# Optimization experiments

Hardware: AMD Instinct MI355X
Metric: run time of the kernel (lower is better)

The kernel has to match this reference:

```python
import jax, jax.numpy as jnp
import numpy as np

HEADS = 16
IN_FEATURE = 1024
D_HEAD = IN_FEATURE // HEADS
N = 32768


def setup_inputs() -> dict:
    key = jax.random.key(0)
    ks = jax.random.split(key, 16)
    s_in = 1.0 / np.sqrt(IN_FEATURE)
    inp = {
        "Q": jax.random.normal(ks[0], (N, IN_FEATURE), jnp.float32),
        "K": jax.random.normal(ks[1], (N, IN_FEATURE), jnp.float32),
        "V": jax.random.normal(ks[2], (N, IN_FEATURE), jnp.float32),
        "lq_w": jax.random.uniform(ks[3], (D_HEAD, IN_FEATURE), jnp.float32, -s_in, s_in),
        "lq_b": jax.random.uniform(ks[4], (D_HEAD,), jnp.float32, -s_in, s_in),
        "lk1_w": jax.random.uniform(ks[5], (D_HEAD, IN_FEATURE), jnp.float32, -s_in, s_in),
        "lk1_b": jax.random.uniform(ks[6], (D_HEAD,), jnp.float32, -s_in, s_in),
        "lk2_w": jax.random.uniform(ks[7], (D_HEAD, IN_FEATURE), jnp.float32, -s_in, s_in),
        "lk2_b": jax.random.uniform(ks[8], (D_HEAD,), jnp.float32, -s_in, s_in),
        "lv1_w": jax.random.uniform(ks[9], (D_HEAD, IN_FEATURE), jnp.float32, -s_in, s_in),
        "lv1_b": jax.random.uniform(ks[10], (D_HEAD,), jnp.float32, -s_in, s_in),
        "lv2_w": jax.random.uniform(ks[11], (D_HEAD, IN_FEATURE), jnp.float32, -s_in, s_in),
        "lv2_b": jax.random.uniform(ks[12], (D_HEAD,), jnp.float32, -s_in, s_in),
        "lh_w": jax.random.uniform(ks[13], (IN_FEATURE, IN_FEATURE), jnp.float32, -s_in, s_in),
        "lh_b": jax.random.uniform(ks[14], (IN_FEATURE,), jnp.float32, -s_in, s_in),
    }
    return inp


def _linear(x, w, b):
    # torch nn.Linear: x @ w.T + b
    return x @ w.T + b


def reference(Q, K, V, lq_w, lq_b, lk1_w, lk1_b, lk2_w, lk2_b,
              lv1_w, lv1_b, lv2_w, lv2_b, lh_w, lh_b):
    # The original loops over heads but the body is loop-invariant:
    # every iteration produces the identical [N, D_HEAD] tensor.
    # Compute once and tile HEADS times (same math as the torch code).
    q = _linear(Q, lq_w, lq_b)     # [N, Dh]
    k1 = _linear(K, lk1_w, lk1_b)  # [N, Dh]
    k2 = _linear(V, lk2_w, lk2_b)
    v1 = _linear(K, lv1_w, lv1_b)
    v2 = _linear(V, lv2_w, lv2_b)

    kv1 = jnp.sum(q * k1, axis=1, keepdims=True)  # [N, 1]
    kv2 = jnp.sum(q * k2, axis=1, keepdims=True)  # [N, 1]
    m = jnp.maximum(kv1, kv2)
    e1 = jnp.exp(kv1 - m)
    e2 = jnp.exp(kv2 - m)
    denom = e1 + e2
    head = (e1 / denom) * v1 + (e2 / denom) * v2   # [N, Dh]

    concat_head = jnp.tile(head, (1, HEADS))       # [N, IN_FEATURE]
    return _linear(concat_head, lh_w, lh_b)
```

## Files before the change

### kernel.cpp

```cpp
#include <hip/hip_runtime.h>
#include <hip/hip_bf16.h>

typedef __attribute__((ext_vector_type(4))) float f32x4;
typedef __attribute__((ext_vector_type(8))) short bf16x8;

#define MFMA(a, b, c) __builtin_amdgcn_mfma_f32_16x16x32_bf16(a, b, c, 0, 0, 0)

__device__ __forceinline__ short f2bf(float f) {
    union { float f; unsigned u; } v; v.f = f;
    unsigned r = v.u + 0x7fffu + ((v.u >> 16) & 1u);
    return (short)(r >> 16);
}

__device__ __forceinline__ short f2bf_h(float f) {
    __hip_bfloat16 h = __float2bfloat16(f);
    return *reinterpret_cast<const short*>(&h);
}

__device__ __forceinline__ bf16x8 cvt8h(f32x4 a, f32x4 b) {
    bf16x8 r;
    #pragma unroll
    for (int i = 0; i < 4; ++i) {
        r[i]     = f2bf_h(a[i]);
        r[4 + i] = f2bf_h(b[i]);
    }
    return r;
}

__device__ __forceinline__ void gll16(const void* g, const void* l) {
    __builtin_amdgcn_global_load_lds(
        (const __attribute__((address_space(1))) void*)g,
        (__attribute__((address_space(3))) void*)l, 16, 0, 0);
}

#define WS_WEFF   327680
#define WS_BALL_B 786432

__global__ __launch_bounds__(256) void prep_kernel(
        const float* __restrict__ lq_w, const float* __restrict__ lk1_w,
        const float* __restrict__ lk2_w, const float* __restrict__ lv1_w,
        const float* __restrict__ lv2_w, const float* __restrict__ lh_w,
        const float* __restrict__ lq_b, const float* __restrict__ lk1_b,
        const float* __restrict__ lk2_b, const float* __restrict__ lv1_b,
        const float* __restrict__ lv2_b,
        short* __restrict__ W_frag, short* __restrict__ weff,
        float* __restrict__ b_all) {
    int t = blockIdx.x * 256 + threadIdx.x;
    if (t < 327680) {
        const int e    = t & 7;
        const int u16  = t >> 3;
        const int lane = u16 & 63;
        const int tl   = u16 >> 6;
        const int c    = tl / 20;
        const int tt   = tl - c * 20;
        const int j    = tt >> 2;
        const int wd   = tt & 3;
        const int lrow = lane & 15;
        const int lkg  = lane >> 4;
        const float* src = (j == 0) ? lq_w : (j == 1) ? lk1_w
                         : (j == 2) ? lv1_w : (j == 3) ? lk2_w : lv2_w;
        W_frag[t] = f2bf(src[(wd * 16 + lrow) * 1024 + c * 32 + lkg * 8 + e]);
    } else if (t < 393216) {
        int i = t - 327680;
        int jj = i >> 6, d = i & 63;
        float s = 0.f;
        #pragma unroll
        for (int h = 0; h < 16; ++h) s += lh_w[jj * 1024 + h * 64 + d];
        weff[i] = f2bf(s);
    } else if (t < 393536) {
        int i = t - 393216;
        int seg = i >> 6, si = i & 63;
        const float* src = (seg == 0) ? lq_b : (seg == 1) ? lk1_b
                         : (seg == 2) ? lv1_b : (seg == 3) ? lk2_b : lv2_b;
        b_all[i] = src[si];
    }
}

__global__ __launch_bounds__(256, 3) void fused_kernel(
        const float* __restrict__ Q, const float* __restrict__ K,
        const float* __restrict__ V, const short* __restrict__ W_frag,
        const float* __restrict__ b_all, const short* __restrict__ weff,
        const float* __restrict__ lh_b, float* __restrict__ out) {
    __shared__ __align__(16) char lds[49152];
    const int tid  = threadIdx.x;
    const int wid  = tid >> 6;
    const int lane = tid & 63;
    const int lrow = lane & 15;
    const int lkg  = lane >> 4;
    const int RB   = blockIdx.x * 32;

    const float* asrc[3];
    int adst[3];
    #pragma unroll
    for (int u = 0; u < 3; ++u) {
        const int i   = wid * 3 + u;
        const int inp = i >> 2;
        const int rg  = i & 3;
        const int row = rg * 8 + (lane >> 3);
        const int gc  = (lane & 7) ^ (row & 7);
        const float* base = (inp == 0) ? Q : (inp == 1) ? K : V;
        asrc[u] = base + (size_t)(RB + row) * 1024 + gc * 4;
        adst[u] = inp * 4096 + rg * 1024;
    }

    const short* wsrc[5];
    #pragma unroll
    for (int j = 0; j < 5; ++j)
        wsrc[j] = W_frag + (size_t)((j * 4 + wid) * 64 + lane) * 8;

    f32x4 acc[2][5];
    #pragma unroll
    for (int rt = 0; rt < 2; ++rt)
        #pragma unroll
        for (int j = 0; j < 5; ++j) acc[rt][j] = (f32x4){0.f, 0.f, 0.f, 0.f};

    bf16x8 wE[5], wO[5];
    const int r7 = lrow & 7;
    const int c0 = ((lkg * 2)     ^ r7) << 4;
    const int c1 = ((lkg * 2 + 1) ^ r7) << 4;

#define GLD4(dst, p) \
    asm volatile("global_load_dwordx4 %0, %1, off" : "=&v"(dst) : "v"(p) : "memory")

    #pragma unroll
    for (int u = 0; u < 3; ++u) gll16(asrc[u], lds + adst[u]);
    #pragma unroll
    for (int j = 0; j < 5; ++j) GLD4(wE[j], wsrc[j]);
    #pragma unroll
    for (int u = 0; u < 3; ++u) gll16(asrc[u] + 32, lds + 12288 + adst[u]);
    #pragma unroll
    for (int j = 0; j < 5; ++j) GLD4(wO[j], wsrc[j] + 10240);
    #pragma unroll
    for (int u = 0; u < 3; ++u) gll16(asrc[u] + 64, lds + 24576 + adst[u]);
    asm volatile("s_waitcnt vmcnt(11)" ::: "memory");
    __builtin_amdgcn_sched_barrier(0);
    __builtin_amdgcn_s_barrier();
    __builtin_amdgcn_sched_barrier(0);

#define BODY(C, WB)                                                            \
    {                                                                          \
        const char* Ab = lds + ((C) & 3) * 12288;                              \
        bf16x8 fq[2], fk[2], fv[2];                                            \
        _Pragma("unroll")                                                      \
        for (int rt = 0; rt < 2; ++rt) {                                       \
            const int ro = (rt * 16 + lrow) * 128;                             \
            f32x4 q0 = *(const f32x4*)(Ab + ro + c0);                          \
            f32x4 q1 = *(const f32x4*)(Ab + ro + c1);                          \
            f32x4 k0 = *(const f32x4*)(Ab + 4096 + ro + c0);                   \
            f32x4 k1 = *(const f32x4*)(Ab + 4096 + ro + c1);                   \
            f32x4 v0 = *(const f32x4*)(Ab + 8192 + ro + c0);                   \
            f32x4 v1 = *(const f32x4*)(Ab + 8192 + ro + c1);                   \
            fq[rt] = cvt8h(q0, q1);                                            \
            fk[rt] = cvt8h(k0, k1);                                            \
            fv[rt] = cvt8h(v0, v1);                                            \
        }                                                                      \
        _Pragma("unroll")                                                      \
        for (int rt = 0; rt < 2; ++rt) {                                       \
            acc[rt][0] = MFMA(fq[rt], WB[0], acc[rt][0]);                      \
            acc[rt][1] = MFMA(fk[rt], WB[1], acc[rt][1]);                      \
            acc[rt][2] = MFMA(fk[rt], WB[2], acc[rt][2]);                      \
            acc[rt][3] = MFMA(fv[rt], WB[3], acc[rt][3]);                      \
            acc[rt][4] = MFMA(fv[rt], WB[4], acc[rt][4]);                      \
        }                                                                      \
        __builtin_amdgcn_sched_barrier(0);                                     \
           \
        const int kw = ((C) + 2 <= 31) ? (C) + 2 : 31;                         \
        _Pragma("unroll")                                                      \
        for (int j = 0; j < 5; ++j) GLD4(WB[j], wsrc[j] + kw * 10240);         \
               \
        const int ka = ((C) + 3 <= 31) ? (C) + 3 : 31;                         \
        char* Db = lds + (((C) + 3) & 3) * 12288;                              \
        _Pragma("unroll")                                                      \
        for (int u = 0; u < 3; ++u) gll16(asrc[u] + ka * 32, Db + adst[u]);    \
        __builtin_amdgcn_sched_barrier(0);                                     \
        asm volatile("s_waitcnt vmcnt(11)" ::: "memory");                      \
        __builtin_amdgcn_sched_barrier(0);                                     \
        __builtin_amdgcn_s_barrier();                                          \
        __builtin_amdgcn_sched_barrier(0);                                     \
    }

    #pragma unroll 1
    for (int cc = 0; cc < 32; cc += 2) {
        BODY(cc, wE)
        BODY(cc + 1, wO)
    }
#undef BODY
#undef GLD4

    asm volatile("s_waitcnt vmcnt(0)" ::: "memory");
    __builtin_amdgcn_sched_barrier(0);
    __syncthreads();

    float* epi = (float*)lds;
    #pragma unroll
    for (int rt = 0; rt < 2; ++rt)
        #pragma unroll
        for (int j = 0; j < 5; ++j) {
            const int col = j * 64 + wid * 16 + lrow;
            const float bb = b_all[col];
            #pragma unroll
            for (int i = 0; i < 4; ++i)
                epi[(rt * 16 + lkg * 4 + i) * 324 + col] = acc[rt][j][i] + bb;
        }
    __syncthreads();

    const int r = tid >> 3;
    const int p = tid & 7;
    const float* er = epi + r * 324;
    float p1 = 0.f, p2 = 0.f;
    #pragma unroll
    for (int jj = 0; jj < 8; ++jj) {
        const float qv = er[p * 8 + jj];
        p1 += qv * er[64  + p * 8 + jj];
        p2 += qv * er[192 + p * 8 + jj];
    }
    p1 += __shfl_xor(p1, 1, 64); p1 += __shfl_xor(p1, 2, 64); p1 += __shfl_xor(p1, 4, 64);
    p2 += __shfl_xor(p2, 1, 64); p2 += __shfl_xor(p2, 2, 64); p2 += __shfl_xor(p2, 4, 64);
    const float mx = fmaxf(p1, p2);
    const float e1 = __expf(p1 - mx);
    const float e2 = __expf(p2 - mx);
    const float inv = 1.f / (e1 + e2);
    const float g1 = e1 * inv, g2 = e2 * inv;

    short* head_s = (short*)(lds + 41472);
    #pragma unroll
    for (int d = 0; d < 8; ++d) {
        const float h = g1 * er[128 + p * 8 + d] + g2 * er[256 + p * 8 + d];
        head_s[r * 72 + p * 8 + d] = f2bf_h(h);
    }
    __syncthreads();

    bf16x8 ha[2][2];
    #pragma unroll
    for (int rt = 0; rt < 2; ++rt) {
        ha[rt][0] = *(const bf16x8*)(head_s + (rt * 16 + lrow) * 72 + lkg * 8);
        ha[rt][1] = *(const bf16x8*)(head_s + (rt * 16 + lrow) * 72 + 32 + lkg * 8);
    }
    const int cgbase = wid * 256;
    #pragma unroll 4
    for (int jt = 0; jt < 16; ++jt) {
        const int col = cgbase + jt * 16 + lrow;
        const float bb = lh_b[col];
        const short* wp = weff + col * 64 + lkg * 8;
        const bf16x8 w0 = *(const bf16x8*)(wp);
        const bf16x8 w1 = *(const bf16x8*)(wp + 32);
        #pragma unroll
        for (int rt = 0; rt < 2; ++rt) {
            f32x4 a = {bb, bb, bb, bb};
            a = MFMA(ha[rt][0], w0, a);
            a = MFMA(ha[rt][1], w1, a);
            #pragma unroll
            for (int i = 0; i < 4; ++i)
                out[(size_t)(RB + rt * 16 + lkg * 4 + i) * 1024 + col] = a[i];
        }
    }
}

extern "C" void kernel_launch(void* const* d_in, const int* in_sizes, int n_in,
                              void* d_out, int out_size, void* d_ws, size_t ws_size,
                              hipStream_t stream) {
    const float* Q     = (const float*)d_in[0];
    const float* K     = (const float*)d_in[1];
    const float* V     = (const float*)d_in[2];
    const float* lq_w  = (const float*)d_in[3];
    const float* lq_b  = (const float*)d_in[4];
    const float* lk1_w = (const float*)d_in[5];
    const float* lk1_b = (const float*)d_in[6];
    const float* lk2_w = (const float*)d_in[7];
    const float* lk2_b = (const float*)d_in[8];
    const float* lv1_w = (const float*)d_in[9];
    const float* lv1_b = (const float*)d_in[10];
    const float* lv2_w = (const float*)d_in[11];
    const float* lv2_b = (const float*)d_in[12];
    const float* lh_w  = (const float*)d_in[13];
    const float* lh_b  = (const float*)d_in[14];
    float* out = (float*)d_out;

    short* W_frag = (short*)d_ws;
    short* weff   = W_frag + WS_WEFF;
    float* b_all  = (float*)((char*)d_ws + WS_BALL_B);

    prep_kernel<<<1538, 256, 0, stream>>>(lq_w, lk1_w, lk2_w, lv1_w, lv2_w, lh_w,
                                          lq_b, lk1_b, lk2_b, lv1_b, lv2_b,
                                          W_frag, weff, b_all);
    fused_kernel<<<1024, 256, 0, stream>>>(Q, K, V, W_frag, b_all, weff, lh_b, out);
}
```

Measured before the change: 137.3 us.

## Shrink LDS to a three-stage A ring and slim the epilogue staging

```diff
diff --git a/kernel.cpp b/kernel.cpp
--- a/kernel.cpp
+++ b/kernel.cpp
@@ -81,7 +81,7 @@
         const float* __restrict__ V, const short* __restrict__ W_frag,
         const float* __restrict__ b_all, const short* __restrict__ weff,
         const float* __restrict__ lh_b, float* __restrict__ out) {
-    __shared__ __align__(16) char lds[49152];
+    __shared__ __align__(16) char lds[36864];
     const int tid  = threadIdx.x;
     const int wid  = tid >> 6;
     const int lane = tid & 63;
@@ -130,16 +130,15 @@
     for (int u = 0; u < 3; ++u) gll16(asrc[u] + 32, lds + 12288 + adst[u]);
     #pragma unroll
     for (int j = 0; j < 5; ++j) GLD4(wO[j], wsrc[j] + 10240);
-    #pragma unroll
-    for (int u = 0; u < 3; ++u) gll16(asrc[u] + 64, lds + 24576 + adst[u]);
-    asm volatile("s_waitcnt vmcnt(11)" ::: "memory");
+    asm volatile("s_waitcnt vmcnt(8)" ::: "memory");
     __builtin_amdgcn_sched_barrier(0);
     __builtin_amdgcn_s_barrier();
     __builtin_amdgcn_sched_barrier(0);
 
-#define BODY(C, WB)                                                            \
+#define BODY(C, K, WB)                                                         \
     {                                                                          \
-        const char* Ab = lds + ((C) & 3) * 12288;                              \
+             \
+        const char* Ab = lds + (K) % 3 * 12288;                                \
         bf16x8 fq[2], fk[2], fv[2];                                            \
         _Pragma("unroll")                                                      \
         for (int rt = 0; rt < 2; ++rt) {                                       \
@@ -163,27 +162,29 @@
             acc[rt][4] = MFMA(fv[rt], WB[4], acc[rt][4]);                      \
         }                                                                      \
         __builtin_amdgcn_sched_barrier(0);                                     \
-           \
+                \
         const int kw = ((C) + 2 <= 31) ? (C) + 2 : 31;                         \
         _Pragma("unroll")                                                      \
         for (int j = 0; j < 5; ++j) GLD4(WB[j], wsrc[j] + kw * 10240);         \
-               \
-        const int ka = ((C) + 3 <= 31) ? (C) + 3 : 31;                         \
-        char* Db = lds + (((C) + 3) & 3) * 12288;                              \
+                     \
+        const int ka = ((C) + 2 <= 31) ? (C) + 2 : 31;                         \
+        char* Db = lds + ((K) + 2) % 3 * 12288;                                \
         _Pragma("unroll")                                                      \
         for (int u = 0; u < 3; ++u) gll16(asrc[u] + ka * 32, Db + adst[u]);    \
         __builtin_amdgcn_sched_barrier(0);                                     \
-        asm volatile("s_waitcnt vmcnt(11)" ::: "memory");                      \
+        asm volatile("s_waitcnt vmcnt(8)" ::: "memory");                       \
         __builtin_amdgcn_sched_barrier(0);                                     \
         __builtin_amdgcn_s_barrier();                                          \
         __builtin_amdgcn_sched_barrier(0);                                     \
     }
 
     #pragma unroll 1
-    for (int cc = 0; cc < 32; cc += 2) {
-        BODY(cc, wE)
-        BODY(cc + 1, wO)
-    }
+    for (int g = 0; g < 5; ++g) {
+        const int base = g * 6;
+        BODY(base + 0, 0, wE) BODY(base + 1, 1, wO) BODY(base + 2, 2, wE)
+        BODY(base + 3, 3, wO) BODY(base + 4, 4, wE) BODY(base + 5, 5, wO)
+    }
+    BODY(30, 0, wE) BODY(31, 1, wO)
 #undef BODY
 #undef GLD4
 
@@ -191,42 +192,63 @@
     __builtin_amdgcn_sched_barrier(0);
     __syncthreads();
 
-    float* epi = (float*)lds;
-    #pragma unroll
-    for (int rt = 0; rt < 2; ++rt)
-        #pragma unroll
-        for (int j = 0; j < 5; ++j) {
-            const int col = j * 64 + wid * 16 + lrow;
-            const float bb = b_all[col];
+    float* qa  = (float*)lds;
+    float* k1a = qa  + 32 * 65;
+    float* k2a = k1a + 32 * 65;
+    float* g12 = k2a + 32 * 65;
+    short* head_s = (short*)(g12 + 64);
+
+    const int segc = wid * 16 + lrow;
+    #pragma unroll
+    for (int rt = 0; rt < 2; ++rt) {
+        #pragma unroll
+        for (int i = 0; i < 4; ++i) {
+            const int row = rt * 16 + lkg * 4 + i;
+            qa [row * 65 + segc] = acc[rt][0][i] + b_all[segc];
+            k1a[row * 65 + segc] = acc[rt][1][i] + b_all[64 + segc];
+            k2a[row * 65 + segc] = acc[rt][3][i] + b_all[192 + segc];
+        }
+    }
+    __syncthreads();
+
+    {
+        const int r = tid >> 3;
+        const int p = tid & 7;
+        float p1 = 0.f, p2 = 0.f;
+        #pragma unroll
+        for (int jj = 0; jj < 8; ++jj) {
+            const float qv = qa[r * 65 + p * 8 + jj];
+            p1 += qv * k1a[r * 65 + p * 8 + jj];
+            p2 += qv * k2a[r * 65 + p * 8 + jj];
+        }
+        p1 += __shfl_xor(p1, 1, 64); p1 += __shfl_xor(p1, 2, 64); p1 += __shfl_xor(p1, 4, 64);
+        p2 += __shfl_xor(p2, 1, 64); p2 += __shfl_xor(p2, 2, 64); p2 += __shfl_xor(p2, 4, 64);
+        if (p == 0) {
+            const float mx = fmaxf(p1, p2);
+            const float e1 = __expf(p1 - mx);
+            const float e2 = __expf(p2 - mx);
+            const float inv = 1.f / (e1 + e2);
+            g12[r * 2]     = e1 * inv;
+            g12[r * 2 + 1] = e2 * inv;
+        }
+    }
+    __syncthreads();
+
+    {
+        const float bv1 = b_all[128 + segc];
+        const float bv2 = b_all[256 + segc];
+        #pragma unroll
+        for (int rt = 0; rt < 2; ++rt) {
             #pragma unroll
-            for (int i = 0; i < 4; ++i)
-                epi[(rt * 16 + lkg * 4 + i) * 324 + col] = acc[rt][j][i] + bb;
-        }
-    __syncthreads();
-
-    const int r = tid >> 3;
-    const int p = tid & 7;
-    const float* er = epi + r * 324;
-    float p1 = 0.f, p2 = 0.f;
-    #pragma unroll
-    for (int jj = 0; jj < 8; ++jj) {
-        const float qv = er[p * 8 + jj];
-        p1 += qv * er[64  + p * 8 + jj];
-        p2 += qv * er[192 + p * 8 + jj];
-    }
-    p1 += __shfl_xor(p1, 1, 64); p1 += __shfl_xor(p1, 2, 64); p1 += __shfl_xor(p1, 4, 64);
-    p2 += __shfl_xor(p2, 1, 64); p2 += __shfl_xor(p2, 2, 64); p2 += __shfl_xor(p2, 4, 64);
-    const float mx = fmaxf(p1, p2);
-    const float e1 = __expf(p1 - mx);
-    const float e2 = __expf(p2 - mx);
-    const float inv = 1.f / (e1 + e2);
-    const float g1 = e1 * inv, g2 = e2 * inv;
-
-    short* head_s = (short*)(lds + 41472);
-    #pragma unroll
-    for (int d = 0; d < 8; ++d) {
-        const float h = g1 * er[128 + p * 8 + d] + g2 * er[256 + p * 8 + d];
-        head_s[r * 72 + p * 8 + d] = f2bf_h(h);
+            for (int i = 0; i < 4; ++i) {
+                const int row = rt * 16 + lkg * 4 + i;
+                const float g1 = g12[row * 2];
+                const float g2 = g12[row * 2 + 1];
+                const float h = g1 * (acc[rt][2][i] + bv1)
+                              + g2 * (acc[rt][4][i] + bv2);
+                head_s[row * 72 + segc] = f2bf_h(h);
+            }
+        }
     }
     __syncthreads();
 
```

Measured after the change: 150.4 us. 1.1x slower.
